# Kernel optimization log

Hardware: AMD Instinct MI355X
Metric: run time of the kernel (lower is better)

## Reference

```python
import jax, jax.numpy as jnp
import numpy as np

LN_EPS = 1e-5


def layer_norm(x, gamma, beta):
    mu = jnp.mean(x, axis=-1, keepdims=True)
    var = jnp.mean(jnp.square(x - mu), axis=-1, keepdims=True)
    return (x - mu) * jax.lax.rsqrt(var + LN_EPS) * gamma + beta


def setup_inputs() -> dict:
    key = jax.random.key(0)
    ks = jax.random.split(key, 7)
    B, S, D = 8, 1024, 512
    H, Dh = 8, 64
    scale = 1.0 / np.sqrt(D)
    x = jax.random.normal(ks[0], (B, S, D), dtype=jnp.float32)
    Wq = jax.random.normal(ks[1], (D, H * Dh), dtype=jnp.float32) * scale
    Wk = jax.random.normal(ks[2], (D, H * Dh), dtype=jnp.float32) * scale
    Wv = jax.random.normal(ks[3], (D, H * Dh), dtype=jnp.float32) * scale
    Wfc = jax.random.normal(ks[4], (H * Dh, D), dtype=jnp.float32) * scale
    gamma = jnp.ones((D,), dtype=jnp.float32)
    beta = jnp.zeros((D,), dtype=jnp.float32)
    return {"x": x, "Wq": Wq, "Wk": Wk, "Wv": Wv, "Wfc": Wfc, "gamma": gamma, "beta": beta}


def reference(x, Wq, Wk, Wv, Wfc, gamma, beta):
    B, S, D = x.shape
    H, Dh = 8, 64
    Q = (x @ Wq).reshape(B, S, H, Dh).transpose(0, 2, 1, 3)  # [B,H,S,Dh]
    K = (x @ Wk).reshape(B, S, H, Dh).transpose(0, 2, 1, 3)
    V = (x @ Wv).reshape(B, S, H, Dh).transpose(0, 2, 1, 3)
    scores = jnp.einsum('bhqd,bhkd->bhqk', Q, K) / np.sqrt(Dh).astype(np.float32)
    # tridiagonal band mask; NOTE: original fills off-band with -1e-09 (not -inf)
    idx = jnp.arange(S)
    band = jnp.abs(idx[:, None] - idx[None, :]) <= 1  # [S,S]
    scores = jnp.where(band, scores, jnp.float32(-1e-09))
    attn = jax.nn.softmax(scores, axis=-1)
    context = jnp.einsum('bhqk,bhkd->bhqd', attn, V)  # [B,H,S,Dh]
    context = context.transpose(0, 2, 1, 3).reshape(B, S, H * Dh)
    out = context @ Wfc
    return layer_norm(out + x, gamma, beta)
```

## Files before the change

### kernel.cpp

```cpp
#include <hip/hip_runtime.h>
#include <math.h>


typedef short     s8v  __attribute__((ext_vector_type(8)));
typedef float     f4v  __attribute__((ext_vector_type(4)));
typedef unsigned short us4v __attribute__((ext_vector_type(4)));
typedef unsigned short us8v __attribute__((ext_vector_type(8)));

__device__ __forceinline__ unsigned short f2b(float f) {
  union { float f; unsigned int u; } v; v.f = f;
  unsigned int u = v.u;
  return (unsigned short)((u + 0x7fffu + ((u >> 16) & 1u)) >> 16);
}
__device__ __forceinline__ float b2f(unsigned short u) {
  union { unsigned int i; float f; } v; v.i = ((unsigned int)u) << 16;
  return v.f;
}
__device__ __forceinline__ void gload_lds16(const void* g, void* l) {
  __builtin_amdgcn_global_load_lds(
      (const __attribute__((address_space(1))) void*)g,
      (__attribute__((address_space(3))) void*)l, 16, 0, 0);
}

__global__ __launch_bounds__(256) void conv_kernel(
    const float* __restrict__ x,
    const float* __restrict__ Wq, const float* __restrict__ Wk,
    const float* __restrict__ Wv, const float* __restrict__ Wfc,
    unsigned short* __restrict__ xb, unsigned short* __restrict__ Wt,
    float* __restrict__ Vsum) {
  __shared__ unsigned short tile[32][33];
  const int bid = blockIdx.x, t = threadIdx.x;
  if (bid < 4096) {
    const int i = bid * 256 + t;
    const float4 f = ((const float4*)x)[i];
    us4v o; o[0] = f2b(f.x); o[1] = f2b(f.y); o[2] = f2b(f.z); o[3] = f2b(f.w);
    ((us4v*)xb)[i] = o;
  } else if (bid < 5120) {
    const int id = bid - 4096;
    const int z = id >> 8, rem = id & 255;
    const int bx = rem & 15, by = rem >> 4;
    const float* W = (z == 0) ? Wq : (z == 1) ? Wk : (z == 2) ? Wv : Wfc;
    const int tx = t & 31, ty = t >> 5;
    const int n0 = bx * 32, k0 = by * 32;
    #pragma unroll
    for (int r = ty; r < 32; r += 8)
      tile[r][tx] = f2b(W[(size_t)(k0 + r) * 512 + n0 + tx]);
    __syncthreads();
    unsigned short* dst = Wt + (size_t)z * 512 * 512;
    #pragma unroll
    for (int r = ty; r < 32; r += 8)
      dst[(size_t)(n0 + r) * 512 + k0 + tx] = tile[tx][r];
  } else {
    float4 zz = {0.f, 0.f, 0.f, 0.f};
    #pragma unroll
    for (int p = 0; p < 4; ++p) ((float4*)Vsum)[p * 256 + t] = zz;
  }
}

__global__ __launch_bounds__(256) void gemm_qkv_kernel(
    const unsigned short* __restrict__ A, const unsigned short* __restrict__ Bt,
    unsigned short* __restrict__ C, float* __restrict__ Vsum) {
  const int N = 1536, K = 512;
  __shared__ __align__(16) unsigned short smem[16384];
  unsigned short* As = smem;
  unsigned short* Bs = smem + 8192;
  const int t = threadIdx.x, wave = t >> 6, lane = t & 63;
  const int wr = wave >> 1, wc = wave & 1;
  const int quad = lane >> 4, l16 = lane & 15;
  const int bm = blockIdx.y * 128, bn = blockIdx.x * 128;

  const unsigned short *gA[4], *gB[4];
  #pragma unroll
  for (int p = 0; p < 4; ++p) {
    const int ci = wave * 256 + p * 64 + lane;
    const int r = ci >> 3, c = (ci & 7) ^ (r & 7);
    gA[p] = A + (size_t)(bm + r) * K + c * 8;
    gB[p] = Bt + (size_t)(bn + r) * K + c * 8;
  }

  f4v acc[4][4];
  #pragma unroll
  for (int i = 0; i < 4; ++i)
    #pragma unroll
    for (int j = 0; j < 4; ++j) {
      f4v z = {0.f, 0.f, 0.f, 0.f};
      acc[i][j] = z;
    }

  #pragma unroll
  for (int it = 0; it < 8; ++it) {
    const int kt = it * 64;
    #pragma unroll
    for (int p = 0; p < 4; ++p)
      gload_lds16(gA[p] + kt, As + wave * 2048 + p * 512);
    #pragma unroll
    for (int p = 0; p < 4; ++p)
      gload_lds16(gB[p] + kt, Bs + wave * 2048 + p * 512);
    __syncthreads();

    #pragma unroll
    for (int s = 0; s < 2; ++s) {
      s8v af[4], bf[4];
      #pragma unroll
      for (int i = 0; i < 4; ++i) {
        const int r = wr * 64 + i * 16 + l16;
        af[i] = *(const s8v*)&As[(r * 8 + ((quad + 4 * s) ^ (r & 7))) * 8];
      }
      #pragma unroll
      for (int j = 0; j < 4; ++j) {
        const int r = wc * 64 + j * 16 + l16;
        bf[j] = *(const s8v*)&Bs[(r * 8 + ((quad + 4 * s) ^ (r & 7))) * 8];
      }
      #pragma unroll
      for (int i = 0; i < 4; ++i)
        #pragma unroll
        for (int j = 0; j < 4; ++j)
          acc[i][j] = __builtin_amdgcn_mfma_f32_16x16x32_bf16(
              af[i], bf[j], acc[i][j], 0, 0, 0);
    }
    __syncthreads();
  }

  if (bn >= 1024) {
    const int b = bm >> 10;
    #pragma unroll
    for (int j = 0; j < 4; ++j) {
      float ps = 0.f;
      #pragma unroll
      for (int i = 0; i < 4; ++i)
        #pragma unroll
        for (int r = 0; r < 4; ++r) ps += acc[i][j][r];
      ps += __shfl_xor(ps, 16);
      ps += __shfl_xor(ps, 32);
      if (quad == 0)
        atomicAdd(&Vsum[b * 512 + (bn - 1024) + wc * 64 + j * 16 + l16], ps);
    }
  }

  #pragma unroll
  for (int i = 0; i < 4; ++i) {
    const int lr0 = wr * 64 + i * 16 + quad * 4;
    #pragma unroll
    for (int j = 0; j < 4; ++j) {
      const int lc = wc * 64 + j * 16 + l16;
      #pragma unroll
      for (int r = 0; r < 4; ++r)
        smem[(lr0 + r) * 128 + lc] = f2b(acc[i][j][r]);
    }
  }
  __syncthreads();
  #pragma unroll
  for (int p = 0; p < 8; ++p) {
    const int row = p * 16 + (t >> 4);
    const int ch  = t & 15;
    *(us8v*)(C + (size_t)(bm + row) * N + bn + ch * 8) =
        *(const us8v*)&smem[row * 128 + ch * 8];
  }
}

#define OS 516

__global__ __launch_bounds__(512) void attn_fcln_kernel(
    const unsigned short* __restrict__ QKV,
    const float* __restrict__ Vsum,
    const unsigned short* __restrict__ Bt,
    const unsigned short* __restrict__ xb, const float* __restrict__ gamma,
    const float* __restrict__ beta, float* __restrict__ y) {
  const int K = 512;
  __shared__ __align__(16) unsigned short smem[81920];
  unsigned short* ctxS = smem + 65536;
  float* outS = (float*)smem;

  const int t = threadIdx.x, wave = t >> 6, lane = t & 63;
  const int bm = blockIdx.x * 32;

  const unsigned short* gB[8];
  #pragma unroll
  for (int p = 0; p < 8; ++p) {
    const int ci = wave * 512 + p * 64 + lane;
    const int r = ci >> 3, c = (ci & 7) ^ (r & 7);
    gB[p] = Bt + (size_t)r * K + c * 8;
  }
  #pragma unroll
  for (int p = 0; p < 8; ++p)
    gload_lds16(gB[p], smem + wave * 4096 + p * 512);

  {
    const int ql   = t >> 4;
    const int h    = (t >> 1) & 7;
    const int half = t & 1;
    const int b    = bm >> 10;
    const int qq   = (bm & 1023) + ql;
    const int co   = h * 64 + half * 32;
    const size_t rowb = (size_t)b * 1024 * 1536;
    const int qm = qq > 0 ? qq - 1 : 0;
    const int qp = qq < 1023 ? qq + 1 : 1023;
    const unsigned short* Qp  = QKV + rowb + (size_t)qq * 1536 + co;
    const unsigned short* Kp0 = QKV + rowb + (size_t)qq * 1536 + 512 + co;
    const unsigned short* Kpm = QKV + rowb + (size_t)qm * 1536 + 512 + co;
    const unsigned short* Kpp = QKV + rowb + (size_t)qp * 1536 + 512 + co;

    us8v qv[4], km[4], k0[4], kp[4];
    #pragma unroll
    for (int j = 0; j < 4; ++j) {
      qv[j] = *(const us8v*)(Qp  + j * 8);
      km[j] = *(const us8v*)(Kpm + j * 8);
      k0[j] = *(const us8v*)(Kp0 + j * 8);
      kp[j] = *(const us8v*)(Kpp + j * 8);
    }
    float pm = 0.f, p0 = 0.f, pp = 0.f;
    #pragma unroll
    for (int j = 0; j < 4; ++j)
      #pragma unroll
      for (int r = 0; r < 8; ++r) {
        const float qf = b2f(qv[j][r]);
        pm += qf * b2f(km[j][r]);
        p0 += qf * b2f(k0[j][r]);
        pp += qf * b2f(kp[j][r]);
      }
    pm += __shfl_xor(pm, 1);
    p0 += __shfl_xor(p0, 1);
    pp += __shfl_xor(pp, 1);

    const float OFF = -1e-9f;
    const float s0 = p0 * 0.125f;
    const float sm = (qq > 0)    ? pm * 0.125f : OFF;
    const float sp = (qq < 1023) ? pp * 0.125f : OFF;
    const float m  = fmaxf(fmaxf(s0, sm), fmaxf(sp, OFF));
    const float e0 = __expf(s0 - m), em = __expf(sm - m), ep = __expf(sp - m);
    const float eoff = __expf(OFF - m);
    const float inv  = 1.f / (e0 + em + ep + 1021.f * eoff);
    const float wm = (em - eoff) * inv, w0 = (e0 - eoff) * inv,
                wp = (ep - eoff) * inv, wt = eoff * inv;

    const unsigned short* Vp0 = Kp0 + 512;
    const unsigned short* Vpm = Kpm + 512;
    const unsigned short* Vpp = Kpp + 512;
    const float* vsp = Vsum + b * 512 + co;
    us8v o[4];
    #pragma unroll
    for (int jj = 0; jj < 4; ++jj) {
      const us8v a  = *(const us8v*)(Vpm + jj * 8);
      const us8v v0 = *(const us8v*)(Vp0 + jj * 8);
      const us8v c  = *(const us8v*)(Vpp + jj * 8);
      const float4 vsa = *(const float4*)&vsp[jj * 8];
      const float4 vsb = *(const float4*)&vsp[jj * 8 + 4];
      #pragma unroll
      for (int r = 0; r < 4; ++r) {
        const float vs0 = (&vsa.x)[r];
        const float vs1 = (&vsb.x)[r];
        o[jj][r]     = f2b(wt * vs0 + wm * b2f(a[r]) + w0 * b2f(v0[r]) +
                           wp * b2f(c[r]));
        o[jj][r + 4] = f2b(wt * vs1 + wm * b2f(a[r + 4]) + w0 * b2f(v0[r + 4]) +
                           wp * b2f(c[r + 4]));
      }
    }
    #pragma unroll
    for (int s = 0; s < 4; ++s) {
      const int jj = (s + h) & 3;
      const int ch = (co >> 3) + jj;
      const int slot = (ch & 56) | ((ch & 7) ^ (ql & 7));
      *(us8v*)&ctxS[ql * 512 + slot * 8] = o[jj];
    }
  }
  __syncthreads();

  const int wrr = wave >> 2, wcc = wave & 3;
  const int quad = lane >> 4, l16 = lane & 15;

  f4v acc[8];
  #pragma unroll
  for (int j = 0; j < 8; ++j) {
    f4v z = {0.f, 0.f, 0.f, 0.f};
    acc[j] = z;
  }

  #pragma unroll
  for (int it = 0; it < 8; ++it) {
    const int cur = (it & 1) * 32768;
    const int nxt = 32768 - cur;
    const unsigned short* Bb = smem + cur;
    const int rm = wrr * 16 + l16;
    const s8v af0 =
        *(const s8v*)&ctxS[rm * 512 + (it * 8 + (quad ^ (rm & 7))) * 8];
    const s8v af1 =
        *(const s8v*)&ctxS[rm * 512 + (it * 8 + ((quad + 4) ^ (rm & 7))) * 8];
    s8v bf0[8];
    #pragma unroll
    for (int j = 0; j < 8; ++j) {
      const int n = wcc * 128 + j * 16 + l16;
      bf0[j] = *(const s8v*)&Bb[(n * 8 + (quad ^ (n & 7))) * 8];
    }
    if (it < 7) {
      const int kt = (it + 1) * 64;
      #pragma unroll
      for (int p = 0; p < 8; ++p)
        gload_lds16(gB[p] + kt, smem + nxt + wave * 4096 + p * 512);
    }
    #pragma unroll
    for (int j = 0; j < 8; ++j)
      acc[j] = __builtin_amdgcn_mfma_f32_16x16x32_bf16(af0, bf0[j], acc[j], 0, 0, 0);
    #pragma unroll
    for (int j = 0; j < 8; ++j) {
      const int n = wcc * 128 + j * 16 + l16;
      const s8v bf1 = *(const s8v*)&Bb[(n * 8 + ((quad + 4) ^ (n & 7))) * 8];
      acc[j] = __builtin_amdgcn_mfma_f32_16x16x32_bf16(af1, bf1, acc[j], 0, 0, 0);
    }
    __syncthreads();
  }

  #pragma unroll
  for (int j = 0; j < 8; ++j) {
    const int col = wcc * 128 + j * 16 + l16;
    const int row0 = wrr * 16 + quad * 4;
    #pragma unroll
    for (int r = 0; r < 4; ++r)
      outS[(row0 + r) * OS + col] = acc[j][r];
  }
  __syncthreads();

  const int row = t >> 4, l = t & 15;
  const size_t gbase = (size_t)(bm + row) * 512;
  float4 v[8];
  float s1 = 0.f, s2 = 0.f;
  #pragma unroll
  for (int k = 0; k < 8; ++k) {
    const int c = k * 64 + l * 4;
    const float4 a = *(const float4*)&outS[row * OS + c];
    const us4v xv = *(const us4v*)&xb[gbase + c];
    float4 w;
    w.x = a.x + b2f(xv[0]); w.y = a.y + b2f(xv[1]);
    w.z = a.z + b2f(xv[2]); w.w = a.w + b2f(xv[3]);
    v[k] = w;
    s1 += w.x + w.y + w.z + w.w;
    s2 += w.x * w.x + w.y * w.y + w.z * w.z + w.w * w.w;
  }
  #pragma unroll
  for (int m = 1; m < 16; m <<= 1) {
    s1 += __shfl_xor(s1, m);
    s2 += __shfl_xor(s2, m);
  }
  const float mu  = s1 * (1.f / 512.f);
  const float var = s2 * (1.f / 512.f) - mu * mu;
  const float rs  = rsqrtf(var + 1e-5f);
  #pragma unroll
  for (int k = 0; k < 8; ++k) {
    const int c = k * 64 + l * 4;
    const float4 g  = *(const float4*)&gamma[c];
    const float4 bb = *(const float4*)&beta[c];
    float4 o;
    o.x = (v[k].x - mu) * rs * g.x + bb.x;
    o.y = (v[k].y - mu) * rs * g.y + bb.y;
    o.z = (v[k].z - mu) * rs * g.z + bb.z;
    o.w = (v[k].w - mu) * rs * g.w + bb.w;
    *(float4*)&y[gbase + c] = o;
  }
}

extern "C" void kernel_launch(void* const* d_in, const int* in_sizes, int n_in,
                              void* d_out, int out_size, void* d_ws, size_t ws_size,
                              hipStream_t stream) {
  const float* x     = (const float*)d_in[0];
  const float* Wq    = (const float*)d_in[1];
  const float* Wk    = (const float*)d_in[2];
  const float* Wv    = (const float*)d_in[3];
  const float* Wfc   = (const float*)d_in[4];
  const float* gamma = (const float*)d_in[5];
  const float* beta  = (const float*)d_in[6];
  float* y = (float*)d_out;

  char* ws = (char*)d_ws;
  unsigned short* Wt   = (unsigned short*)(ws);
  unsigned short* xb   = (unsigned short*)(ws + 2097152);
  unsigned short* QKV  = (unsigned short*)(ws + 10485760);
  float*          Vsum = (float*)(ws + 35651584);

  conv_kernel<<<5121, 256, 0, stream>>>(x, Wq, Wk, Wv, Wfc, xb, Wt, Vsum);
  gemm_qkv_kernel<<<dim3(12, 64), 256, 0, stream>>>(xb, Wt, QKV, Vsum);
  attn_fcln_kernel<<<256, 512, 0, stream>>>(
      QKV, Vsum, Wt + (size_t)1536 * 512, xb, gamma, beta, y);
}
```

Before: 127.7 us.

## Pipeline per-head band attention computation with the FC MFMA loop

```diff
diff --git a/kernel.cpp b/kernel.cpp
--- a/kernel.cpp
+++ b/kernel.cpp
@@ -158,6 +158,60 @@
   }
 }
 
+__device__ __forceinline__ void attn_load(
+    const unsigned short* __restrict__ QKV, const float* __restrict__ Vsum,
+    size_t oq, size_t om, size_t op, int vsbase, int co,
+    us4v& qv, us4v& km, us4v& k0, us4v& kp,
+    us4v& vm, us4v& v0, us4v& vp, float4& vs) {
+  qv = *(const us4v*)(QKV + oq + co);
+  km = *(const us4v*)(QKV + om + 512 + co);
+  k0 = *(const us4v*)(QKV + oq + 512 + co);
+  kp = *(const us4v*)(QKV + op + 512 + co);
+  vm = *(const us4v*)(QKV + om + 1024 + co);
+  v0 = *(const us4v*)(QKV + oq + 1024 + co);
+  vp = *(const us4v*)(QKV + op + 1024 + co);
+  vs = *(const float4*)(Vsum + vsbase + co);
+}
+
+__device__ __forceinline__ void attn_compute(
+    int qq, int arow, int al, int h, unsigned short* ctxS,
+    us4v qv, us4v km, us4v k0, us4v kp,
+    us4v vm, us4v v0, us4v vp, float4 vs) {
+  float pm = 0.f, p0 = 0.f, pp = 0.f;
+  #pragma unroll
+  for (int r = 0; r < 4; ++r) {
+    const float qf = b2f(qv[r]);
+    pm += qf * b2f(km[r]);
+    p0 += qf * b2f(k0[r]);
+    pp += qf * b2f(kp[r]);
+  }
+  #pragma unroll
+  for (int m = 1; m < 16; m <<= 1) {
+    pm += __shfl_xor(pm, m);
+    p0 += __shfl_xor(p0, m);
+    pp += __shfl_xor(pp, m);
+  }
+  const float OFF = -1e-9f;
+  const float s0 = p0 * 0.125f;
+  const float sm = (qq > 0)    ? pm * 0.125f : OFF;
+  const float sp = (qq < 1023) ? pp * 0.125f : OFF;
+  const float mx = fmaxf(fmaxf(s0, sm), fmaxf(sp, OFF));
+  const float e0 = __expf(s0 - mx), em = __expf(sm - mx), ep = __expf(sp - mx);
+  const float eoff = __expf(OFF - mx);
+  const float inv  = 1.f / (e0 + em + ep + 1021.f * eoff);
+  const float wm = (em - eoff) * inv, w0 = (e0 - eoff) * inv,
+              wp = (ep - eoff) * inv, wt = eoff * inv;
+  us4v o;
+  const float* vsf = (const float*)&vs;
+  #pragma unroll
+  for (int r = 0; r < 4; ++r)
+    o[r] = f2b(wt * vsf[r] + wm * b2f(vm[r]) + w0 * b2f(v0[r]) +
+               wp * b2f(vp[r]));
+  const int ch   = h * 8 + (al >> 1);
+  const int slot = (ch & 56) | ((ch & 7) ^ (arow & 7));
+  *(us4v*)&ctxS[arow * 512 + slot * 8 + (al & 1) * 4] = o;
+}
+
 #define OS 516
 
 __global__ __launch_bounds__(512) void attn_fcln_kernel(
@@ -181,87 +235,26 @@
     const int r = ci >> 3, c = (ci & 7) ^ (r & 7);
     gB[p] = Bt + (size_t)r * K + c * 8;
   }
-  #pragma unroll
-  for (int p = 0; p < 8; ++p)
-    gload_lds16(gB[p], smem + wave * 4096 + p * 512);
+
+  const int arow = t >> 4, al = t & 15;
+  const int b = bm >> 10;
+  const int qq = (bm & 1023) + arow;
+  const int qm = qq > 0 ? qq - 1 : 0;
+  const int qp = qq < 1023 ? qq + 1 : 1023;
+  const size_t rowb = (size_t)b * 1024 * 1536;
+  const size_t oq = rowb + (size_t)qq * 1536;
+  const size_t om = rowb + (size_t)qm * 1536;
+  const size_t op = rowb + (size_t)qp * 1536;
+  const int vsbase = b * 512;
 
   {
-    const int ql   = t >> 4;
-    const int h    = (t >> 1) & 7;
-    const int half = t & 1;
-    const int b    = bm >> 10;
-    const int qq   = (bm & 1023) + ql;
-    const int co   = h * 64 + half * 32;
-    const size_t rowb = (size_t)b * 1024 * 1536;
-    const int qm = qq > 0 ? qq - 1 : 0;
-    const int qp = qq < 1023 ? qq + 1 : 1023;
-    const unsigned short* Qp  = QKV + rowb + (size_t)qq * 1536 + co;
-    const unsigned short* Kp0 = QKV + rowb + (size_t)qq * 1536 + 512 + co;
-    const unsigned short* Kpm = QKV + rowb + (size_t)qm * 1536 + 512 + co;
-    const unsigned short* Kpp = QKV + rowb + (size_t)qp * 1536 + 512 + co;
-
-    us8v qv[4], km[4], k0[4], kp[4];
-    #pragma unroll
-    for (int j = 0; j < 4; ++j) {
-      qv[j] = *(const us8v*)(Qp  + j * 8);
-      km[j] = *(const us8v*)(Kpm + j * 8);
-      k0[j] = *(const us8v*)(Kp0 + j * 8);
-      kp[j] = *(const us8v*)(Kpp + j * 8);
-    }
-    float pm = 0.f, p0 = 0.f, pp = 0.f;
-    #pragma unroll
-    for (int j = 0; j < 4; ++j)
-      #pragma unroll
-      for (int r = 0; r < 8; ++r) {
-        const float qf = b2f(qv[j][r]);
-        pm += qf * b2f(km[j][r]);
-        p0 += qf * b2f(k0[j][r]);
-        pp += qf * b2f(kp[j][r]);
-      }
-    pm += __shfl_xor(pm, 1);
-    p0 += __shfl_xor(p0, 1);
-    pp += __shfl_xor(pp, 1);
-
-    const float OFF = -1e-9f;
-    const float s0 = p0 * 0.125f;
-    const float sm = (qq > 0)    ? pm * 0.125f : OFF;
-    const float sp = (qq < 1023) ? pp * 0.125f : OFF;
-    const float m  = fmaxf(fmaxf(s0, sm), fmaxf(sp, OFF));
-    const float e0 = __expf(s0 - m), em = __expf(sm - m), ep = __expf(sp - m);
-    const float eoff = __expf(OFF - m);
-    const float inv  = 1.f / (e0 + em + ep + 1021.f * eoff);
-    const float wm = (em - eoff) * inv, w0 = (e0 - eoff) * inv,
-                wp = (ep - eoff) * inv, wt = eoff * inv;
-
-    const unsigned short* Vp0 = Kp0 + 512;
-    const unsigned short* Vpm = Kpm + 512;
-    const unsigned short* Vpp = Kpp + 512;
-    const float* vsp = Vsum + b * 512 + co;
-    us8v o[4];
-    #pragma unroll
-    for (int jj = 0; jj < 4; ++jj) {
-      const us8v a  = *(const us8v*)(Vpm + jj * 8);
-      const us8v v0 = *(const us8v*)(Vp0 + jj * 8);
-      const us8v c  = *(const us8v*)(Vpp + jj * 8);
-      const float4 vsa = *(const float4*)&vsp[jj * 8];
-      const float4 vsb = *(const float4*)&vsp[jj * 8 + 4];
-      #pragma unroll
-      for (int r = 0; r < 4; ++r) {
-        const float vs0 = (&vsa.x)[r];
-        const float vs1 = (&vsb.x)[r];
-        o[jj][r]     = f2b(wt * vs0 + wm * b2f(a[r]) + w0 * b2f(v0[r]) +
-                           wp * b2f(c[r]));
-        o[jj][r + 4] = f2b(wt * vs1 + wm * b2f(a[r + 4]) + w0 * b2f(v0[r + 4]) +
-                           wp * b2f(c[r + 4]));
-      }
-    }
-    #pragma unroll
-    for (int s = 0; s < 4; ++s) {
-      const int jj = (s + h) & 3;
-      const int ch = (co >> 3) + jj;
-      const int slot = (ch & 56) | ((ch & 7) ^ (ql & 7));
-      *(us8v*)&ctxS[ql * 512 + slot * 8] = o[jj];
-    }
+    us4v qv, km, k0, kp, vm, v0, vp; float4 vs;
+    attn_load(QKV, Vsum, oq, om, op, vsbase, al * 4,
+              qv, km, k0, kp, vm, v0, vp, vs);
+    #pragma unroll
+    for (int p = 0; p < 8; ++p)
+      gload_lds16(gB[p], smem + wave * 4096 + p * 512);
+    attn_compute(qq, arow, al, 0, ctxS, qv, km, k0, kp, vm, v0, vp, vs);
   }
   __syncthreads();
 
@@ -280,6 +273,12 @@
     const int cur = (it & 1) * 32768;
     const int nxt = 32768 - cur;
     const unsigned short* Bb = smem + cur;
+
+    us4v qv, km, k0, kp, vm, v0, vp; float4 vs;
+    if (it < 7)
+      attn_load(QKV, Vsum, oq, om, op, vsbase, (it + 1) * 64 + al * 4,
+                qv, km, k0, kp, vm, v0, vp, vs);
+
     const int rm = wrr * 16 + l16;
     const s8v af0 =
         *(const s8v*)&ctxS[rm * 512 + (it * 8 + (quad ^ (rm & 7))) * 8];
@@ -306,6 +305,8 @@
       const s8v bf1 = *(const s8v*)&Bb[(n * 8 + ((quad + 4) ^ (n & 7))) * 8];
       acc[j] = __builtin_amdgcn_mfma_f32_16x16x32_bf16(af1, bf1, acc[j], 0, 0, 0);
     }
+    if (it < 7)
+      attn_compute(qq, arow, al, it + 1, ctxS, qv, km, k0, kp, vm, v0, vp, vs);
     __syncthreads();
   }
 
```

Result: faster. 121.4 us (-4.9%).
